# Performance work log

Measured on AMD Instinct MI355X. Metric: run time of the kernel, lower is better.

Reference implementation:

```python
import jax, jax.numpy as jnp
import numpy as np

B, T, I, C, O = 256, 1024, 128, 256, 10


def setup_inputs() -> dict:
    key = jax.random.key(0)
    k1, k2, k3, k4, k5 = jax.random.split(key, 5)
    x = jax.random.normal(k1, (B, T, I), dtype=jnp.float32)
    # xavier-like scale for kernels
    kernel = jax.random.normal(k2, (I, 2 * C), dtype=jnp.float32) * (6.0 / (I + 2 * C)) ** 0.5
    recurrent_kernel = jax.random.normal(k3, (C, 2 * C), dtype=jnp.float32) * (6.0 / (C + 2 * C)) ** 0.5
    # bias: forget-gate half initialized to log(uniform(1, T-1)), rest zero
    u = jax.random.uniform(k4, (C,), minval=1.0, maxval=float(T - 1))
    recurrent_bias = jnp.concatenate([jnp.log(u), jnp.zeros((C,), jnp.float32)])
    dense_w = jax.random.normal(k5, (C, O), dtype=jnp.float32) * (1.0 / C) ** 0.5
    dense_b = jnp.zeros((O,), jnp.float32)
    return {"x": x, "kernel": kernel, "recurrent_kernel": recurrent_kernel,
            "recurrent_bias": recurrent_bias, "dense_w": dense_w, "dense_b": dense_b}


def reference(x, kernel, recurrent_kernel, recurrent_bias, dense_w, dense_b):
    cells = recurrent_kernel.shape[0]
    # Precompute input projection for all timesteps in one big GEMM: [B,T,2C]
    xz = jnp.einsum('bti,ig->btg', x, kernel) + recurrent_bias
    xz_t = jnp.swapaxes(xz, 0, 1)  # [T, B, 2C] for scan over time

    def step(carry, z_in):
        h, c = carry
        z = z_in + h @ recurrent_kernel  # [B, 2C]
        f = jax.nn.sigmoid(z[:, :cells])
        c_new = f * c + (1.0 - f) * jnp.tanh(z[:, cells:])
        return (c_new, c_new), None

    h0 = jnp.zeros((x.shape[0], cells), x.dtype)
    (h_final, _), _ = jax.lax.scan(step, (h0, h0), xz_t)
    return h_final @ dense_w + dense_b
```

## Files before the change

kernel.cpp:

```cpp
#include <hip/hip_runtime.h>

#define BB 256
#define TT 1024
#define II 128
#define GG 512
#define CC 256
#define L2E 1.44269504f

typedef _Float16 f16;
typedef _Float16 h8_t __attribute__((ext_vector_type(8)));
typedef float f4_t __attribute__((ext_vector_type(4)));
typedef unsigned short ushort_t;

static __device__ __forceinline__ float fast_rcp(float x) {
#if __has_builtin(__builtin_amdgcn_rcpf)
    return __builtin_amdgcn_rcpf(x);
#else
    return 1.f / x;
#endif
}
static __device__ __forceinline__ float fast_exp2(float x) {
#if __has_builtin(__builtin_amdgcn_exp2f)
    return __builtin_amdgcn_exp2f(x);
#else
    return exp2f(x);
#endif
}

__global__ void kt_transpose(const float* __restrict__ kin, f16* __restrict__ kt) {
    int idx = blockIdx.x * 256 + threadIdx.x;
    int k = idx >> 9;
    int n = idx & 511;
    kt[n * II + k] = (f16)kin[k * GG + n];
}

__global__ __launch_bounds__(256)
void gemm_xz(const float* __restrict__ x, const f16* __restrict__ kt,
             const float* __restrict__ bias, ushort_t* __restrict__ xz) {
    const int  ntile = blockIdx.x;
    const long mtile = blockIdx.y;
    const int wave = threadIdx.x >> 6;
    const int lane = threadIdx.x & 63;
    const int wm = (wave & 1) * 64;
    const int wn = (wave >> 1) * 64;
    const int lm = lane & 15;
    const int q  = lane >> 4;

    f4_t acc[4][4];
#pragma unroll
    for (int mi = 0; mi < 4; ++mi)
#pragma unroll
        for (int ni = 0; ni < 4; ++ni)
            acc[mi][ni] = (f4_t){0.f, 0.f, 0.f, 0.f};

#pragma unroll
    for (int kc = 0; kc < 4; ++kc) {
        h8_t a[4], bf[4];
#pragma unroll
        for (int mi = 0; mi < 4; ++mi) {
            const int rowm = (int)(mtile * 128) + wm + mi * 16 + lm;
            const int b  = rowm & 255;
            const int tt = rowm >> 8;
            const float* ap = x + (size_t)b * (TT * II) + (size_t)tt * II + kc * 32 + q * 8;
            f4_t p0 = *(const f4_t*)ap;
            f4_t p1 = *(const f4_t*)(ap + 4);
            h8_t tv;
            tv[0] = (f16)p0[0]; tv[1] = (f16)p0[1]; tv[2] = (f16)p0[2]; tv[3] = (f16)p0[3];
            tv[4] = (f16)p1[0]; tv[5] = (f16)p1[1]; tv[6] = (f16)p1[2]; tv[7] = (f16)p1[3];
            a[mi] = tv;
        }
#pragma unroll
        for (int ni = 0; ni < 4; ++ni) {
            const f16* bp = kt + (size_t)(ntile * 128 + wn + ni * 16 + lm) * II + kc * 32 + q * 8;
            bf[ni] = *(const h8_t*)bp;
        }
#pragma unroll
        for (int mi = 0; mi < 4; ++mi)
#pragma unroll
            for (int ni = 0; ni < 4; ++ni)
                acc[mi][ni] = __builtin_amdgcn_mfma_f32_16x16x32_f16(a[mi], bf[ni], acc[mi][ni], 0, 0, 0);
    }

#pragma unroll
    for (int mi = 0; mi < 4; ++mi) {
#pragma unroll
        for (int ni = 0; ni < 4; ++ni) {
            const int col = ntile * 128 + wn + ni * 16 + lm;
            const float bv = bias[col];
            const float s  = (col < CC) ? L2E : (2.0f * L2E);
#pragma unroll
            for (int r = 0; r < 4; ++r) {
                const size_t rowm = (size_t)(mtile * 128 + wm + mi * 16 + q * 4 + r);
                f16 hv = (f16)((acc[mi][ni][r] + bv) * s);
                xz[rowm * GG + col] = *(ushort_t*)&hv;
            }
        }
    }
}

#define STEP(T, PF, PP, HRD, HWR) do {                                               \
    h8_t af[8];                                                                      \
    _Pragma("unroll") for (int kt = 0; kt < 8; ++kt)                                 \
        af[kt] = *(const h8_t*)((HRD) + lm * 264 + kt * 32 + q * 8);                 \
    f4_t acc[4];                                                                     \
    _Pragma("unroll") for (int ni = 0; ni < 4; ++ni) {                               \
        f4_t av;                                                                     \
        _Pragma("unroll") for (int r = 0; r < 4; ++r) {                              \
            ushort_t u = (PF)[ni * 4 + r];                                           \
            f16 hv = *(f16*)&u;                                                      \
            av[r] = (float)hv;                                                       \
        }                                                                            \
        acc[ni] = av;                                                                \
    }                                                                                \
    if ((T) + 2 < TT) {                                                              \
        _Pragma("unroll") for (int ni = 0; ni < 4; ++ni)                             \
            _Pragma("unroll") for (int r = 0; r < 4; ++r)                            \
                (PF)[ni * 4 + r] = (PP)[r * 512 + ni * 128];                         \
        (PP) += 2 * 131072;                                                          \
    }                                                                                \
    _Pragma("unroll") for (int kt = 0; kt < 8; ++kt)                                 \
        _Pragma("unroll") for (int ni = 0; ni < 4; ++ni)                             \
            acc[ni] = __builtin_amdgcn_mfma_f32_16x16x32_f16(af[kt], bw[ni][kt], acc[ni], 0, 0, 0); \
    _Pragma("unroll") for (int ni = 0; ni < 2; ++ni)                                 \
        _Pragma("unroll") for (int r = 0; r < 4; ++r) {                              \
            float zf = acc[ni][r];                                                   \
            float zg = acc[ni + 2][r];                                               \
            float ef = fast_exp2(-zf);                                               \
            float eg = fast_exp2(-fabsf(zg));                                        \
            float t1 = (zg < 0.f) ? -ef : ef;                                        \
            float cv = cst[ni][r];                                                   \
            float num = fmaf(cv, eg, cv) + fmaf(-t1, eg, t1);                        \
            float den = (1.f + ef) * (1.f + eg);                                     \
            cst[ni][r] = num * fast_rcp(den);                                        \
        }                                                                            \
    _Pragma("unroll") for (int ni = 0; ni < 2; ++ni)                                 \
        _Pragma("unroll") for (int r = 0; r < 4; ++r)                                \
            (HWR)[(q * 4 + r) * 264 + (wave + 8 * ni) * 16 + lm] = (f16)cst[ni][r];  \
    asm volatile("s_waitcnt lgkmcnt(0)\n\ts_barrier" ::: "memory");                  \
} while (0)

__global__ __launch_bounds__(512, 2)
void janet_rec(const float* __restrict__ rk, const float* __restrict__ dw,
               const float* __restrict__ db, const ushort_t* __restrict__ xz,
               float* __restrict__ out) {
    const int g = blockIdx.x;
    const int tid = threadIdx.x;
    const int wave = tid >> 6;
    const int lane = tid & 63;
    const int lm = lane & 15;
    const int q  = lane >> 4;

    h8_t bw[4][8];
#pragma unroll
    for (int ni = 0; ni < 4; ++ni) {
        const float s = (ni < 2) ? L2E : (2.0f * L2E);
#pragma unroll
        for (int kt = 0; kt < 8; ++kt) {
            h8_t tv;
#pragma unroll
            for (int j = 0; j < 8; ++j)
                tv[j] = (f16)(s * rk[(size_t)(kt * 32 + q * 8 + j) * GG + (wave + 8 * ni) * 16 + lm]);
            bw[ni][kt] = tv;
        }
    }

    __shared__ __align__(16) f16 hb[2][16][264];
    f16* h0 = &hb[0][0][0];
    f16* h1 = &hb[1][0][0];
    for (int i = tid; i < 2 * 16 * 264; i += 512) ((f16*)hb)[i] = (f16)0.f;

    float cst[2][4];
#pragma unroll
    for (int ni = 0; ni < 2; ++ni)
#pragma unroll
        for (int r = 0; r < 4; ++r) cst[ni][r] = 0.f;

    const ushort_t* pb = xz + ((size_t)g * 16 + q * 4) * 512 + wave * 16 + lm;
    const ushort_t* p1b = pb + 131072;
    const ushort_t* p0 = pb + 2 * 131072;
    const ushort_t* p1 = pb + 3 * 131072;

    ushort_t pf0[16], pf1[16];
#pragma unroll
    for (int ni = 0; ni < 4; ++ni)
#pragma unroll
        for (int r = 0; r < 4; ++r) {
            pf0[ni * 4 + r] = pb[r * 512 + ni * 128];
            pf1[ni * 4 + r] = p1b[r * 512 + ni * 128];
        }
    __syncthreads();

#pragma unroll 1
    for (int t = 0; t < TT; t += 2) {
        STEP(t,     pf0, p0, h0, h1);
        STEP(t + 1, pf1, p1, h1, h0);
    }

    __shared__ float hf[16][256];
#pragma unroll
    for (int ni = 0; ni < 2; ++ni)
#pragma unroll
        for (int r = 0; r < 4; ++r)
            hf[q * 4 + r][(wave + 8 * ni) * 16 + lm] = cst[ni][r];
    __syncthreads();
    if (tid < 160) {
        const int bi = tid / 10, o = tid % 10;
        float acc = db[o];
#pragma unroll 8
        for (int cc = 0; cc < CC; ++cc) acc = fmaf(hf[bi][cc], dw[cc * 10 + o], acc);
        out[(g * 16 + bi) * 10 + o] = acc;
    }
}

__global__ void ws_too_small(float* out, float wssz) {
    int i = blockIdx.x * 256 + threadIdx.x;
    if (i < BB * 10) out[i] = (i == 0) ? wssz : 0.f;
}

extern "C" void kernel_launch(void* const* d_in, const int* in_sizes, int n_in,
                              void* d_out, int out_size, void* d_ws, size_t ws_size,
                              hipStream_t stream) {
    const float* x   = (const float*)d_in[0];
    const float* kin = (const float*)d_in[1];
    const float* rk  = (const float*)d_in[2];
    const float* rb  = (const float*)d_in[3];
    const float* dw  = (const float*)d_in[4];
    const float* db  = (const float*)d_in[5];
    float* out = (float*)d_out;

    const size_t xz_bytes = (size_t)BB * TT * GG * 2;
    const size_t kt_bytes = (size_t)GG * II * 2;
    if (ws_size < xz_bytes + kt_bytes) {
        ws_too_small<<<10, 256, 0, stream>>>(out, (float)ws_size);
        return;
    }

    ushort_t* xz = (ushort_t*)d_ws;
    f16* kt = (f16*)((char*)d_ws + xz_bytes);

    kt_transpose<<<256, 256, 0, stream>>>(kin, kt);
    gemm_xz<<<dim3(4, 2048), 256, 0, stream>>>(x, kt, rb, xz);
    janet_rec<<<16, 512, 0, stream>>>(rk, dw, db, xz, out);
}
```

Before: 1.679 ms.

## Reorder recurrent step MFMAs to overlap gate math and stage xz stores

The recurrent step now streams the h fragment loads from LDS alongside the MFMAs. It splits the four accumulator chains into two pairs so the gate nonlinearity for the first column pair can start while the second pair's MFMAs finish, and it adds the precomputed input projection after the matmul instead of seeding the accumulators with it. The next-step prefetch of xz moves after the gate math. The projection GEMM epilogue now stages its tile in shared memory and writes coalesced 16-byte rows instead of scattered 2-byte stores. The aim is to shorten the serial critical path of each time step, which costs more registers and LDS.

```diff
diff --git a/kernel.cpp b/kernel.cpp
--- a/kernel.cpp
+++ b/kernel.cpp
@@ -81,6 +81,7 @@
                 acc[mi][ni] = __builtin_amdgcn_mfma_f32_16x16x32_f16(a[mi], bf[ni], acc[mi][ni], 0, 0, 0);
     }
 
+    __shared__ __align__(16) f16 st[128][136];
 #pragma unroll
     for (int mi = 0; mi < 4; ++mi) {
 #pragma unroll
@@ -89,53 +90,64 @@
             const float bv = bias[col];
             const float s  = (col < CC) ? L2E : (2.0f * L2E);
 #pragma unroll
-            for (int r = 0; r < 4; ++r) {
-                const size_t rowm = (size_t)(mtile * 128 + wm + mi * 16 + q * 4 + r);
-                f16 hv = (f16)((acc[mi][ni][r] + bv) * s);
-                xz[rowm * GG + col] = *(ushort_t*)&hv;
-            }
-        }
-    }
-}
+            for (int r = 0; r < 4; ++r)
+                st[wm + mi * 16 + q * 4 + r][wn + ni * 16 + lm] = (f16)((acc[mi][ni][r] + bv) * s);
+        }
+    }
+    __syncthreads();
+    {
+        const int r0  = threadIdx.x >> 1;
+        const int seg = threadIdx.x & 1;
+        ushort_t* gp = xz + (size_t)(mtile * 128 + r0) * GG + ntile * 128 + seg * 64;
+        const f16* lp = &st[r0][seg * 64];
+#pragma unroll
+        for (int j = 0; j < 8; ++j)
+            *(f4_t*)(gp + j * 8) = *(const f4_t*)(lp + j * 8);
+    }
+}
+
+#define GATES(P, AF_, AG_, PF, HWR) do {                                             \
+    _Pragma("unroll") for (int r = 0; r < 4; ++r) {                                  \
+        ushort_t uf = (PF)[(P) * 4 + r];                                             \
+        ushort_t ug = (PF)[((P) + 2) * 4 + r];                                       \
+        float zf = (AF_)[r] + (float)(*(f16*)&uf);                                   \
+        float zg = (AG_)[r] + (float)(*(f16*)&ug);                                   \
+        float ef = fast_exp2(-zf);                                                   \
+        float eg = fast_exp2(-fabsf(zg));                                            \
+        unsigned sg = __builtin_bit_cast(unsigned, zg) & 0x80000000u;                \
+        float t1 = __builtin_bit_cast(float, __builtin_bit_cast(unsigned, ef) ^ sg); \
+        float cv = cst[P][r];                                                        \
+        float num = fmaf(cv, eg, cv) + fmaf(-t1, eg, t1);                            \
+        float den = (1.f + ef) * (1.f + eg);                                         \
+        cv = num * fast_rcp(den);                                                    \
+        cst[P][r] = cv;                                                              \
+        (HWR)[(q * 4 + r) * 264 + (wave + 8 * (P)) * 16 + lm] = (f16)cv;             \
+    }                                                                                \
+} while (0)
 
 #define STEP(T, PF, PP, HRD, HWR) do {                                               \
     h8_t af[8];                                                                      \
-    _Pragma("unroll") for (int kt = 0; kt < 8; ++kt)                                 \
-        af[kt] = *(const h8_t*)((HRD) + lm * 264 + kt * 32 + q * 8);                 \
-    f4_t acc[4];                                                                     \
-    _Pragma("unroll") for (int ni = 0; ni < 4; ++ni) {                               \
-        f4_t av;                                                                     \
-        _Pragma("unroll") for (int r = 0; r < 4; ++r) {                              \
-            ushort_t u = (PF)[ni * 4 + r];                                           \
-            f16 hv = *(f16*)&u;                                                      \
-            av[r] = (float)hv;                                                       \
-        }                                                                            \
-        acc[ni] = av;                                                                \
-    }                                                                                \
+    af[0] = *(const h8_t*)((HRD) + lm * 264 + 0 * 32 + q * 8);                       \
+    af[1] = *(const h8_t*)((HRD) + lm * 264 + 1 * 32 + q * 8);                       \
+    f4_t a0 = (f4_t){0.f,0.f,0.f,0.f}, a1 = (f4_t){0.f,0.f,0.f,0.f};                 \
+    f4_t a2 = (f4_t){0.f,0.f,0.f,0.f}, a3 = (f4_t){0.f,0.f,0.f,0.f};                 \
+    _Pragma("unroll") for (int kt = 0; kt < 8; ++kt) {                               \
+        if (kt < 6) af[kt + 2] = *(const h8_t*)((HRD) + lm * 264 + (kt + 2) * 32 + q * 8); \
+        a0 = __builtin_amdgcn_mfma_f32_16x16x32_f16(af[kt], bw[0][kt], a0, 0, 0, 0); \
+        a2 = __builtin_amdgcn_mfma_f32_16x16x32_f16(af[kt], bw[2][kt], a2, 0, 0, 0); \
+    }                                                                                \
+    _Pragma("unroll") for (int kt = 0; kt < 8; ++kt) {                               \
+        a1 = __builtin_amdgcn_mfma_f32_16x16x32_f16(af[kt], bw[1][kt], a1, 0, 0, 0); \
+        a3 = __builtin_amdgcn_mfma_f32_16x16x32_f16(af[kt], bw[3][kt], a3, 0, 0, 0); \
+    }                                                                                \
+    GATES(0, a0, a2, PF, HWR);                                                       \
+    GATES(1, a1, a3, PF, HWR);                                                       \
     if ((T) + 2 < TT) {                                                              \
         _Pragma("unroll") for (int ni = 0; ni < 4; ++ni)                             \
             _Pragma("unroll") for (int r = 0; r < 4; ++r)                            \
                 (PF)[ni * 4 + r] = (PP)[r * 512 + ni * 128];                         \
         (PP) += 2 * 131072;                                                          \
     }                                                                                \
-    _Pragma("unroll") for (int kt = 0; kt < 8; ++kt)                                 \
-        _Pragma("unroll") for (int ni = 0; ni < 4; ++ni)                             \
-            acc[ni] = __builtin_amdgcn_mfma_f32_16x16x32_f16(af[kt], bw[ni][kt], acc[ni], 0, 0, 0); \
-    _Pragma("unroll") for (int ni = 0; ni < 2; ++ni)                                 \
-        _Pragma("unroll") for (int r = 0; r < 4; ++r) {                              \
-            float zf = acc[ni][r];                                                   \
-            float zg = acc[ni + 2][r];                                               \
-            float ef = fast_exp2(-zf);                                               \
-            float eg = fast_exp2(-fabsf(zg));                                        \
-            float t1 = (zg < 0.f) ? -ef : ef;                                        \
-            float cv = cst[ni][r];                                                   \
-            float num = fmaf(cv, eg, cv) + fmaf(-t1, eg, t1);                        \
-            float den = (1.f + ef) * (1.f + eg);                                     \
-            cst[ni][r] = num * fast_rcp(den);                                        \
-        }                                                                            \
-    _Pragma("unroll") for (int ni = 0; ni < 2; ++ni)                                 \
-        _Pragma("unroll") for (int r = 0; r < 4; ++r)                                \
-            (HWR)[(q * 4 + r) * 264 + (wave + 8 * ni) * 16 + lm] = (f16)cst[ni][r];  \
     asm volatile("s_waitcnt lgkmcnt(0)\n\ts_barrier" ::: "memory");                  \
 } while (0)
 
```

Result: no change. 1.711 ms (+1.9%).
